# Performance work log

Hardware: AMD Instinct MI355X
Metric: run time of the kernel (lower is better)

## Reference

```python
import jax, jax.numpy as jnp
import numpy as np

PATCH = 16
EMBED = 384
BINS = 32
LN_EPS = 1e-5


def setup_inputs() -> dict:
    key = jax.random.key(0)
    k1, k2 = jax.random.split(key, 2)
    images = jax.random.uniform(k1, (64, 3, 224, 224), dtype=jnp.float32)  # pixels in [0,1]
    proj_w = jax.random.normal(k2, (EMBED, 3, PATCH, PATCH), dtype=jnp.float32) * 0.02  # OIHW
    proj_b = jnp.zeros((EMBED,), jnp.float32)
    ln_gamma = jnp.ones((EMBED,), jnp.float32)
    ln_beta = jnp.zeros((EMBED,), jnp.float32)
    return {"images": images, "proj_w": proj_w, "proj_b": proj_b,
            "ln_gamma": ln_gamma, "ln_beta": ln_beta}


def _patch_entropy(images, patch_size):
    # images: (B, C, H, W) in [0,1]
    B, C, H, W = images.shape
    gH, gW = H // patch_size, W // patch_size
    gray = images.mean(axis=1)  # (B, H, W)
    # non-overlapping patches -> (B, N, P*P)
    patches = gray.reshape(B, gH, patch_size, gW, patch_size)
    patches = patches.transpose(0, 1, 3, 2, 4).reshape(B, gH * gW, patch_size * patch_size)
    # quantize to 32 bins (floor, matching torch .long() on non-negative values)
    q = jnp.clip(patches * (BINS - 1), 0, BINS - 1).astype(jnp.int32)
    one_hot = jax.nn.one_hot(q, BINS, dtype=jnp.float32)      # (B, N, P*P, 32)
    hist = one_hot.sum(axis=2)                                 # (B, N, 32)
    prob = hist / jnp.maximum(hist.sum(axis=-1, keepdims=True), 1e-8)
    log_prob = jnp.log2(prob + 1e-10)
    entropy = -(prob * log_prob).sum(axis=-1)                  # (B, N)
    return entropy / np.float32(np.log2(BINS))


def reference(images, proj_w, proj_b, ln_gamma, ln_beta):
    p = PATCH
    B, C, H, W = images.shape
    gH, gW = H // p, W // p
    entropy = _patch_entropy(images, p)
    # patch-embed conv: kernel=stride=patch_size, VALID padding
    x = jax.lax.conv_general_dilated(
        images, proj_w, window_strides=(p, p), padding='VALID',
        dimension_numbers=('NCHW', 'OIHW', 'NCHW'))            # (B, D, gH, gW)
    x = x + proj_b[None, :, None, None]
    x = x.transpose(0, 2, 3, 1).reshape(B, gH * gW, -1)        # (B, N, D)
    mu = x.mean(axis=-1, keepdims=True)
    var = x.var(axis=-1, keepdims=True)                        # biased, like torch LayerNorm
    x = (x - mu) / jnp.sqrt(var + LN_EPS) * ln_gamma + ln_beta
    return x, entropy
```

## Files before the change

kernel.cpp:

```cpp
#include <hip/hip_runtime.h>

#define BATCH 64
#define GH 14
#define GW 14
#define NPATCH (GH*GW)
#define M_ROWS (BATCH*NPATCH)
#define KDIM 768
#define DDIM 384
#define HW (224*224)

typedef __attribute__((ext_vector_type(8))) short s16x8;
typedef __attribute__((ext_vector_type(4))) float f32x4;
typedef __attribute__((ext_vector_type(4))) unsigned short u16x4;

__device__ __forceinline__ unsigned short f2bf(float f) {
    unsigned int u = __float_as_uint(f);
    u += 0x7fff + ((u >> 16) & 1);
    return (unsigned short)(u >> 16);
}

__device__ __forceinline__ void load_lds16(const void* g, void* l) {
    __builtin_amdgcn_global_load_lds(
        (const __attribute__((address_space(1))) unsigned int*)g,
        (__attribute__((address_space(3))) unsigned int*)l, 16, 0, 0);
}

__global__ __launch_bounds__(256) void wcast_kernel(const float* __restrict__ w,
                                                    unsigned short* __restrict__ W) {
    int t = blockIdx.x * 256 + threadIdx.x;
    float4 v = ((const float4*)w)[t];
    u16x4 o = { f2bf(v.x), f2bf(v.y), f2bf(v.z), f2bf(v.w) };
    *(u16x4*)(W + t * 4) = o;
}

__global__ __launch_bounds__(256) void patch_kernel(const float* __restrict__ img,
                                                    unsigned short* __restrict__ A,
                                                    float* __restrict__ ent) {
    __shared__ int hist[4][32];
    const int lane = threadIdx.x & 63;
    const int wave = threadIdx.x >> 6;
    const int p = blockIdx.x * 4 + wave;
    const int b = p / NPATCH;
    const int n = p - b * NPATCH;
    const int ph = n / GW, pw = n - ph * GW;

    if (lane < 32) hist[wave][lane] = 0;
    __syncthreads();

    const int r = lane >> 2;
    const int cc = (lane & 3) * 4;
    const float* base = img + (size_t)b * (3 * HW) + (ph * 16 + r) * 224 + pw * 16 + cc;

    float4 v0 = *(const float4*)(base);
    float4 v1 = *(const float4*)(base + HW);
    float4 v2 = *(const float4*)(base + 2 * HW);

    unsigned short* arow = A + (size_t)p * KDIM;
    u16x4 o0 = { f2bf(v0.x), f2bf(v0.y), f2bf(v0.z), f2bf(v0.w) };
    u16x4 o1 = { f2bf(v1.x), f2bf(v1.y), f2bf(v1.z), f2bf(v1.w) };
    u16x4 o2 = { f2bf(v2.x), f2bf(v2.y), f2bf(v2.z), f2bf(v2.w) };
    *(u16x4*)(arow + 0 * 256 + lane * 4) = o0;
    *(u16x4*)(arow + 1 * 256 + lane * 4) = o1;
    *(u16x4*)(arow + 2 * 256 + lane * 4) = o2;

    float g[4] = { (v0.x + v1.x + v2.x) / 3.0f,
                   (v0.y + v1.y + v2.y) / 3.0f,
                   (v0.z + v1.z + v2.z) / 3.0f,
                   (v0.w + v1.w + v2.w) / 3.0f };
#pragma unroll
    for (int j = 0; j < 4; ++j) {
        int bin = (int)(g[j] * 31.0f);
        bin = bin < 0 ? 0 : (bin > 31 ? 31 : bin);
        atomicAdd(&hist[wave][bin], 1);
    }
    __syncthreads();

    float t = 0.0f;
    if (lane < 32) {
        float pr = (float)hist[wave][lane] * (1.0f / 256.0f);
        t = -pr * log2f(pr + 1e-10f);
    }
#pragma unroll
    for (int off = 32; off; off >>= 1) t += __shfl_xor(t, off);
    if (lane == 0) ent[p] = t * (1.0f / 5.0f);
}

__global__ __launch_bounds__(64) void gemm_kernel(const unsigned short* __restrict__ A,
                                                  const unsigned short* __restrict__ Bt,
                                                  const float* __restrict__ bias,
                                                  float* __restrict__ C) {
    __shared__ __align__(16) unsigned short As[64 * 64];
    __shared__ __align__(16) unsigned short Bs[64 * 64];
    const int lane = threadIdx.x;
    const int rowBase = blockIdx.y * 64;
    const int colBase = blockIdx.x * 64;

    f32x4 acc[4][4] = {};

    for (int kt = 0; kt < KDIM; kt += 64) {
#pragma unroll
        for (int i = 0; i < 8; ++i) {
            int f = i * 64 + lane;
            int r = f >> 3, ks = f & 7;
            load_lds16(A  + (size_t)(rowBase + r) * KDIM + kt + ks * 8, (unsigned short*)As + f * 8);
            load_lds16(Bt + (size_t)(colBase + r) * KDIM + kt + ks * 8, (unsigned short*)Bs + f * 8);
        }
        __syncthreads();
#pragma unroll
        for (int ks = 0; ks < 2; ++ks) {
            const int ko = ks * 32 + (lane >> 4) * 8;
            s16x8 a_frag[4], b_frag[4];
#pragma unroll
            for (int i = 0; i < 4; ++i) {
                a_frag[i] = *(const s16x8*)(As + (i * 16 + (lane & 15)) * 64 + ko);
                b_frag[i] = *(const s16x8*)(Bs + (i * 16 + (lane & 15)) * 64 + ko);
            }
#pragma unroll
            for (int i = 0; i < 4; ++i)
#pragma unroll
                for (int j = 0; j < 4; ++j)
                    acc[i][j] = __builtin_amdgcn_mfma_f32_16x16x32_bf16(
                        a_frag[i], b_frag[j], acc[i][j], 0, 0, 0);
        }
        __syncthreads();
    }

    const int quad = lane >> 4;
    const int cl = lane & 15;
#pragma unroll
    for (int j = 0; j < 4; ++j) {
        int col = colBase + j * 16 + cl;
        float bv = bias[col];
#pragma unroll
        for (int i = 0; i < 4; ++i) {
            int row0 = rowBase + i * 16 + quad * 4;
#pragma unroll
            for (int r = 0; r < 4; ++r)
                C[(size_t)(row0 + r) * DDIM + col] = acc[i][j][r] + bv;
        }
    }
}

__global__ __launch_bounds__(256) void ln_kernel(float* __restrict__ X,
                                                 const float* __restrict__ gamma,
                                                 const float* __restrict__ beta) {
    __shared__ float sg[DDIM], sb[DDIM];
    for (int i = threadIdx.x; i < DDIM; i += 256) { sg[i] = gamma[i]; sb[i] = beta[i]; }
    __syncthreads();
    const int lane = threadIdx.x & 63;
    const int wave = threadIdx.x >> 6;
    const int row = blockIdx.x * 4 + wave;
    float* x = X + (size_t)row * DDIM + lane * 6;

    float2 p0 = *(float2*)(x);
    float2 p1 = *(float2*)(x + 2);
    float2 p2 = *(float2*)(x + 4);
    float v[6] = { p0.x, p0.y, p1.x, p1.y, p2.x, p2.y };

    float s = v[0] + v[1] + v[2] + v[3] + v[4] + v[5];
#pragma unroll
    for (int off = 32; off; off >>= 1) s += __shfl_xor(s, off);
    float mean = s * (1.0f / (float)DDIM);

    float d = 0.0f;
#pragma unroll
    for (int j = 0; j < 6; ++j) { float t = v[j] - mean; d += t * t; }
#pragma unroll
    for (int off = 32; off; off >>= 1) d += __shfl_xor(d, off);
    float rstd = 1.0f / sqrtf(d * (1.0f / (float)DDIM) + 1e-5f);

    const float* g = sg + lane * 6;
    const float* b = sb + lane * 6;
#pragma unroll
    for (int j = 0; j < 6; ++j) x[j] = (v[j] - mean) * rstd * g[j] + b[j];
}

extern "C" void kernel_launch(void* const* d_in, const int* in_sizes, int n_in,
                              void* d_out, int out_size, void* d_ws, size_t ws_size,
                              hipStream_t stream) {
    const float* img = (const float*)d_in[0];
    const float* pw  = (const float*)d_in[1];
    const float* pb  = (const float*)d_in[2];
    const float* gam = (const float*)d_in[3];
    const float* bet = (const float*)d_in[4];
    float* out = (float*)d_out;

    unsigned short* Abf = (unsigned short*)d_ws;
    unsigned short* Wbf = (unsigned short*)((char*)d_ws + 19267584);
    float* ent = out + (size_t)M_ROWS * DDIM;

    hipLaunchKernelGGL(wcast_kernel, dim3(288),      dim3(256), 0, stream, pw, Wbf);
    hipLaunchKernelGGL(patch_kernel, dim3(3136),     dim3(256), 0, stream, img, Abf, ent);
    hipLaunchKernelGGL(gemm_kernel,  dim3(6, 196),   dim3(64),  0, stream, Abf, Wbf, pb, out);
    hipLaunchKernelGGL(ln_kernel,    dim3(3136),     dim3(256), 0, stream, out, gam, bet);
}
```

Measured before the change: 123.4 us.

## Fuse LayerNorm into full-width GEMM and merge weight cast into patch kernel

The weight bf16 cast now runs as extra blocks of the patch kernel, and the GEMM is restructured so each 384-thread block computes a full 64x384 row tile. LayerNorm is then applied in the epilogue using shuffle and LDS-atomic row reductions, which removes the fp32 round trip of the output through a separate LN kernel. LDS tiles are XOR-swizzled to avoid bank conflicts. The trade-off is only 196 blocks for the GEMM, which lowers parallelism on a large GPU, plus a one-pass variance computed as E[x^2]-mu^2.

```diff
diff --git a/kernel.cpp b/kernel.cpp
--- a/kernel.cpp
+++ b/kernel.cpp
@@ -25,17 +25,18 @@
         (__attribute__((address_space(3))) unsigned int*)l, 16, 0, 0);
 }
 
-__global__ __launch_bounds__(256) void wcast_kernel(const float* __restrict__ w,
-                                                    unsigned short* __restrict__ W) {
-    int t = blockIdx.x * 256 + threadIdx.x;
-    float4 v = ((const float4*)w)[t];
-    u16x4 o = { f2bf(v.x), f2bf(v.y), f2bf(v.z), f2bf(v.w) };
-    *(u16x4*)(W + t * 4) = o;
-}
-
 __global__ __launch_bounds__(256) void patch_kernel(const float* __restrict__ img,
+                                                    const float* __restrict__ w,
                                                     unsigned short* __restrict__ A,
+                                                    unsigned short* __restrict__ W,
                                                     float* __restrict__ ent) {
+    if (blockIdx.x >= 3136) {
+        int t = (blockIdx.x - 3136) * 256 + threadIdx.x;
+        float4 v = ((const float4*)w)[t];
+        u16x4 o = { f2bf(v.x), f2bf(v.y), f2bf(v.z), f2bf(v.w) };
+        *(u16x4*)(W + t * 4) = o;
+        return;
+    }
     __shared__ int hist[4][32];
     const int lane = threadIdx.x & 63;
     const int wave = threadIdx.x >> 6;
@@ -85,35 +86,57 @@
     if (lane == 0) ent[p] = t * (1.0f / 5.0f);
 }
 
-__global__ __launch_bounds__(64) void gemm_kernel(const unsigned short* __restrict__ A,
-                                                  const unsigned short* __restrict__ Bt,
-                                                  const float* __restrict__ bias,
-                                                  float* __restrict__ C) {
-    __shared__ __align__(16) unsigned short As[64 * 64];
-    __shared__ __align__(16) unsigned short Bs[64 * 64];
-    const int lane = threadIdx.x;
-    const int rowBase = blockIdx.y * 64;
-    const int colBase = blockIdx.x * 64;
+__global__ __launch_bounds__(384) void gemm_ln_kernel(const unsigned short* __restrict__ A,
+                                                      const unsigned short* __restrict__ Bt,
+                                                      const float* __restrict__ bias,
+                                                      const float* __restrict__ gamma,
+                                                      const float* __restrict__ beta,
+                                                      float* __restrict__ C) {
+    __shared__ __align__(16) unsigned short SH[(64 + 384) * 64];
+    __shared__ float sred[64], sred2[64], smean[64], srstd[64];
+    unsigned short* As = SH;
+    unsigned short* Bs = SH + 64 * 64;
+
+    const int tid  = threadIdx.x;
+    const int lane = tid & 63;
+    const int w    = tid >> 6;
+    const int quad = lane >> 4;
+    const int cl   = lane & 15;
+    const int rowBase = blockIdx.x * 64;
+
+    if (tid < 64) { sred[tid] = 0.0f; sred2[tid] = 0.0f; }
 
     f32x4 acc[4][4] = {};
 
     for (int kt = 0; kt < KDIM; kt += 64) {
 #pragma unroll
-        for (int i = 0; i < 8; ++i) {
-            int f = i * 64 + lane;
-            int r = f >> 3, ks = f & 7;
-            load_lds16(A  + (size_t)(rowBase + r) * KDIM + kt + ks * 8, (unsigned short*)As + f * 8);
-            load_lds16(Bt + (size_t)(colBase + r) * KDIM + kt + ks * 8, (unsigned short*)Bs + f * 8);
+        for (int i = 0; i < 10; ++i) {
+            int cb = i * 384 + w * 64;
+            if (i == 9 && cb >= 3584 - 64 + 64) {  }
+            if (i == 9 && w >= 2) break;
+            int c = (i == 9) ? (3456 + tid) : (cb + lane);
+            if (c < 512) {
+                int r  = c >> 3, kss = c & 7;
+                int ksg = kss ^ (r & 7);
+                load_lds16(A + (size_t)(rowBase + r) * KDIM + kt + ksg * 8,
+                           (unsigned short*)SH + c * 8);
+            } else {
+                int cc2 = c - 512;
+                int n  = cc2 >> 3, kss = cc2 & 7;
+                int ksg = kss ^ (n & 7);
+                load_lds16(Bt + (size_t)n * KDIM + kt + ksg * 8,
+                           (unsigned short*)SH + c * 8);
+            }
         }
         __syncthreads();
 #pragma unroll
         for (int ks = 0; ks < 2; ++ks) {
-            const int ko = ks * 32 + (lane >> 4) * 8;
+            const int sw = (ks * 4 + quad) ^ (cl & 7);
             s16x8 a_frag[4], b_frag[4];
 #pragma unroll
             for (int i = 0; i < 4; ++i) {
-                a_frag[i] = *(const s16x8*)(As + (i * 16 + (lane & 15)) * 64 + ko);
-                b_frag[i] = *(const s16x8*)(Bs + (i * 16 + (lane & 15)) * 64 + ko);
+                a_frag[i] = *(const s16x8*)(As + ((i * 16 + cl) * 8 + sw) * 8);
+                b_frag[i] = *(const s16x8*)(Bs + ((w * 64 + i * 16 + cl) * 8 + sw) * 8);
             }
 #pragma unroll
             for (int i = 0; i < 4; ++i)
@@ -125,54 +148,56 @@
         __syncthreads();
     }
 
-    const int quad = lane >> 4;
-    const int cl = lane & 15;
+    float bv[4], gv[4], btv[4];
 #pragma unroll
     for (int j = 0; j < 4; ++j) {
-        int col = colBase + j * 16 + cl;
-        float bv = bias[col];
-#pragma unroll
-        for (int i = 0; i < 4; ++i) {
-            int row0 = rowBase + i * 16 + quad * 4;
-#pragma unroll
-            for (int r = 0; r < 4; ++r)
-                C[(size_t)(row0 + r) * DDIM + col] = acc[i][j][r] + bv;
-        }
-    }
-}
-
-__global__ __launch_bounds__(256) void ln_kernel(float* __restrict__ X,
-                                                 const float* __restrict__ gamma,
-                                                 const float* __restrict__ beta) {
-    __shared__ float sg[DDIM], sb[DDIM];
-    for (int i = threadIdx.x; i < DDIM; i += 256) { sg[i] = gamma[i]; sb[i] = beta[i]; }
-    __syncthreads();
-    const int lane = threadIdx.x & 63;
-    const int wave = threadIdx.x >> 6;
-    const int row = blockIdx.x * 4 + wave;
-    float* x = X + (size_t)row * DDIM + lane * 6;
-
-    float2 p0 = *(float2*)(x);
-    float2 p1 = *(float2*)(x + 2);
-    float2 p2 = *(float2*)(x + 4);
-    float v[6] = { p0.x, p0.y, p1.x, p1.y, p2.x, p2.y };
-
-    float s = v[0] + v[1] + v[2] + v[3] + v[4] + v[5];
-#pragma unroll
-    for (int off = 32; off; off >>= 1) s += __shfl_xor(s, off);
-    float mean = s * (1.0f / (float)DDIM);
-
-    float d = 0.0f;
-#pragma unroll
-    for (int j = 0; j < 6; ++j) { float t = v[j] - mean; d += t * t; }
-#pragma unroll
-    for (int off = 32; off; off >>= 1) d += __shfl_xor(d, off);
-    float rstd = 1.0f / sqrtf(d * (1.0f / (float)DDIM) + 1e-5f);
-
-    const float* g = sg + lane * 6;
-    const float* b = sb + lane * 6;
-#pragma unroll
-    for (int j = 0; j < 6; ++j) x[j] = (v[j] - mean) * rstd * g[j] + b[j];
+        int col = w * 64 + j * 16 + cl;
+        bv[j] = bias[col]; gv[j] = gamma[col]; btv[j] = beta[col];
+    }
+
+#pragma unroll
+    for (int i = 0; i < 4; ++i) {
+#pragma unroll
+        for (int r = 0; r < 4; ++r) {
+            float s1 = 0.0f, s2 = 0.0f;
+#pragma unroll
+            for (int j = 0; j < 4; ++j) {
+                float v = acc[i][j][r] + bv[j];
+                s1 += v; s2 += v * v;
+            }
+#pragma unroll
+            for (int off = 1; off < 16; off <<= 1) {
+                s1 += __shfl_xor(s1, off);
+                s2 += __shfl_xor(s2, off);
+            }
+            if (cl == 0) {
+                int row = i * 16 + quad * 4 + r;
+                atomicAdd(&sred[row], s1);
+                atomicAdd(&sred2[row], s2);
+            }
+        }
+    }
+    __syncthreads();
+    if (tid < 64) {
+        float mu  = sred[tid] * (1.0f / (float)DDIM);
+        float var = sred2[tid] * (1.0f / (float)DDIM) - mu * mu;
+        smean[tid] = mu;
+        srstd[tid] = rsqrtf(var + 1e-5f);
+    }
+    __syncthreads();
+
+#pragma unroll
+    for (int i = 0; i < 4; ++i) {
+#pragma unroll
+        for (int r = 0; r < 4; ++r) {
+            int row = i * 16 + quad * 4 + r;
+            float mu = smean[row], rs = srstd[row];
+            float* crow = C + (size_t)(rowBase + row) * DDIM;
+#pragma unroll
+            for (int j = 0; j < 4; ++j)
+                crow[w * 64 + j * 16 + cl] = (acc[i][j][r] + bv[j] - mu) * rs * gv[j] + btv[j];
+        }
+    }
 }
 
 extern "C" void kernel_launch(void* const* d_in, const int* in_sizes, int n_in,
@@ -189,8 +214,8 @@
     unsigned short* Wbf = (unsigned short*)((char*)d_ws + 19267584);
     float* ent = out + (size_t)M_ROWS * DDIM;
 
-    hipLaunchKernelGGL(wcast_kernel, dim3(288),      dim3(256), 0, stream, pw, Wbf);
-    hipLaunchKernelGGL(patch_kernel, dim3(3136),     dim3(256), 0, stream, img, Abf, ent);
-    hipLaunchKernelGGL(gemm_kernel,  dim3(6, 196),   dim3(64),  0, stream, Abf, Wbf, pb, out);
-    hipLaunchKernelGGL(ln_kernel,    dim3(3136),     dim3(256), 0, stream, out, gam, bet);
-}
+    hipLaunchKernelGGL(patch_kernel,   dim3(3424), dim3(256), 0, stream,
+                       img, pw, Abf, Wbf, ent);
+    hipLaunchKernelGGL(gemm_ln_kernel, dim3(196),  dim3(384), 0, stream,
+                       Abf, Wbf, pb, gam, bet, out);
+}
```

After: 114.4 us. -7.3%, faster.

## Swizzle GEMM LDS tiles and fold weight cast into patch kernel

Applied to the files above, without the earlier changes.

Applies an XOR swizzle to the k-segment index when loading A/B tiles into LDS, and uses the same swizzle on the fragment reads. This is meant to remove bank conflicts on the 128-byte-stride row reads. It also merges the weight bf16 cast into the patch kernel as extra blocks, saving one kernel launch. Division by 3 is replaced with multiplication by the reciprocal, which can change rounding slightly at histogram bin edges.

```diff
diff --git a/kernel.cpp b/kernel.cpp
--- a/kernel.cpp
+++ b/kernel.cpp
@@ -1,10 +1,7 @@
 #include <hip/hip_runtime.h>
 
-#define BATCH 64
-#define GH 14
-#define GW 14
-#define NPATCH (GH*GW)
-#define M_ROWS (BATCH*NPATCH)
+#define NPATCH 196
+#define M_ROWS 12544
 #define KDIM 768
 #define DDIM 384
 #define HW (224*224)
@@ -25,24 +22,25 @@
         (__attribute__((address_space(3))) unsigned int*)l, 16, 0, 0);
 }
 
-__global__ __launch_bounds__(256) void wcast_kernel(const float* __restrict__ w,
-                                                    unsigned short* __restrict__ W) {
-    int t = blockIdx.x * 256 + threadIdx.x;
-    float4 v = ((const float4*)w)[t];
-    u16x4 o = { f2bf(v.x), f2bf(v.y), f2bf(v.z), f2bf(v.w) };
-    *(u16x4*)(W + t * 4) = o;
-}
-
 __global__ __launch_bounds__(256) void patch_kernel(const float* __restrict__ img,
+                                                    const float* __restrict__ w,
                                                     unsigned short* __restrict__ A,
+                                                    unsigned short* __restrict__ W,
                                                     float* __restrict__ ent) {
+    if (blockIdx.x >= 3136) {
+        int t = (blockIdx.x - 3136) * 256 + threadIdx.x;
+        float4 v = ((const float4*)w)[t];
+        u16x4 o = { f2bf(v.x), f2bf(v.y), f2bf(v.z), f2bf(v.w) };
+        *(u16x4*)(W + t * 4) = o;
+        return;
+    }
     __shared__ int hist[4][32];
     const int lane = threadIdx.x & 63;
     const int wave = threadIdx.x >> 6;
     const int p = blockIdx.x * 4 + wave;
     const int b = p / NPATCH;
     const int n = p - b * NPATCH;
-    const int ph = n / GW, pw = n - ph * GW;
+    const int ph = n / 14, pw = n - ph * 14;
 
     if (lane < 32) hist[wave][lane] = 0;
     __syncthreads();
@@ -63,10 +61,10 @@
     *(u16x4*)(arow + 1 * 256 + lane * 4) = o1;
     *(u16x4*)(arow + 2 * 256 + lane * 4) = o2;
 
-    float g[4] = { (v0.x + v1.x + v2.x) / 3.0f,
-                   (v0.y + v1.y + v2.y) / 3.0f,
-                   (v0.z + v1.z + v2.z) / 3.0f,
-                   (v0.w + v1.w + v2.w) / 3.0f };
+    float g[4] = { (v0.x + v1.x + v2.x) * (1.0f / 3.0f),
+                   (v0.y + v1.y + v2.y) * (1.0f / 3.0f),
+                   (v0.z + v1.z + v2.z) * (1.0f / 3.0f),
+                   (v0.w + v1.w + v2.w) * (1.0f / 3.0f) };
 #pragma unroll
     for (int j = 0; j < 4; ++j) {
         int bin = (int)(g[j] * 31.0f);
@@ -92,6 +90,8 @@
     __shared__ __align__(16) unsigned short As[64 * 64];
     __shared__ __align__(16) unsigned short Bs[64 * 64];
     const int lane = threadIdx.x;
+    const int quad = lane >> 4;
+    const int cl   = lane & 15;
     const int rowBase = blockIdx.y * 64;
     const int colBase = blockIdx.x * 64;
 
@@ -101,19 +101,20 @@
 #pragma unroll
         for (int i = 0; i < 8; ++i) {
             int f = i * 64 + lane;
-            int r = f >> 3, ks = f & 7;
-            load_lds16(A  + (size_t)(rowBase + r) * KDIM + kt + ks * 8, (unsigned short*)As + f * 8);
-            load_lds16(Bt + (size_t)(colBase + r) * KDIM + kt + ks * 8, (unsigned short*)Bs + f * 8);
+            int r = f >> 3, kss = f & 7;
+            int ksg = (kss ^ (r & 7)) * 8;
+            load_lds16(A  + (size_t)(rowBase + r) * KDIM + kt + ksg, (unsigned short*)As + f * 8);
+            load_lds16(Bt + (size_t)(colBase + r) * KDIM + kt + ksg, (unsigned short*)Bs + f * 8);
         }
         __syncthreads();
 #pragma unroll
         for (int ks = 0; ks < 2; ++ks) {
-            const int ko = ks * 32 + (lane >> 4) * 8;
+            const int sw = (ks * 4 + quad) ^ (cl & 7);
             s16x8 a_frag[4], b_frag[4];
 #pragma unroll
             for (int i = 0; i < 4; ++i) {
-                a_frag[i] = *(const s16x8*)(As + (i * 16 + (lane & 15)) * 64 + ko);
-                b_frag[i] = *(const s16x8*)(Bs + (i * 16 + (lane & 15)) * 64 + ko);
+                a_frag[i] = *(const s16x8*)(As + (i * 16 + cl) * 64 + sw * 8);
+                b_frag[i] = *(const s16x8*)(Bs + (i * 16 + cl) * 64 + sw * 8);
             }
 #pragma unroll
             for (int i = 0; i < 4; ++i)
@@ -125,8 +126,6 @@
         __syncthreads();
     }
 
-    const int quad = lane >> 4;
-    const int cl = lane & 15;
 #pragma unroll
     for (int j = 0; j < 4; ++j) {
         int col = colBase + j * 16 + cl;
@@ -189,8 +188,10 @@
     unsigned short* Wbf = (unsigned short*)((char*)d_ws + 19267584);
     float* ent = out + (size_t)M_ROWS * DDIM;
 
-    hipLaunchKernelGGL(wcast_kernel, dim3(288),      dim3(256), 0, stream, pw, Wbf);
-    hipLaunchKernelGGL(patch_kernel, dim3(3136),     dim3(256), 0, stream, img, Abf, ent);
-    hipLaunchKernelGGL(gemm_kernel,  dim3(6, 196),   dim3(64),  0, stream, Abf, Wbf, pb, out);
-    hipLaunchKernelGGL(ln_kernel,    dim3(3136),     dim3(256), 0, stream, out, gam, bet);
+    hipLaunchKernelGGL(patch_kernel, dim3(3424),   dim3(256), 0, stream,
+                       img, pw, Abf, Wbf, ent);
+    hipLaunchKernelGGL(gemm_kernel,  dim3(6, 196), dim3(64),  0, stream,
+                       Abf, Wbf, pb, out);
+    hipLaunchKernelGGL(ln_kernel,    dim3(3136),   dim3(256), 0, stream,
+                       out, gam, bet);
 }
```

Result: no change. 121.1 us (-1.9%).
